# Performance work log

Measured on AMD Instinct MI355X. Metric: run time of the kernel, lower is better.

## Reference

```python
import jax, jax.numpy as jnp
import numpy as np

B, S, HID = 32, 577, 768
NH, HD = 12, 64  # num heads, head dim (HID = NH*HD)


def setup_inputs() -> dict:
    key = jax.random.key(0)
    ks = jax.random.split(key, 8)
    scale = 1.0 / np.sqrt(HID)
    return {
        "hidden_states": jax.random.normal(ks[0], (B, S, HID), jnp.float32),
        "lateral_states": jax.random.normal(ks[1], (B, NH, S, HD), jnp.float32),
        "Wq": jax.random.normal(ks[2], (HID, HID), jnp.float32) * scale,
        "bq": jax.random.normal(ks[3], (HID,), jnp.float32) * 0.02,
        "Wk": jax.random.normal(ks[4], (HID, HID), jnp.float32) * scale,
        "bk": jax.random.normal(ks[5], (HID,), jnp.float32) * 0.02,
        "Wv": jax.random.normal(ks[6], (HID, HID), jnp.float32) * scale,
        "bv": jax.random.normal(ks[7], (HID,), jnp.float32) * 0.02,
        "mix_with": 0,  # 0 -> 'q', 1 -> 'k', 2 -> 'v'
    }


def _heads(x):
    # [B, S, HID] -> [B, NH, S, HD]
    return x.reshape(B, S, NH, HD).transpose(0, 2, 1, 3)


def reference(hidden_states, lateral_states, Wq, bq, Wk, bk, Wv, bv, mix_with):
    q = _heads(hidden_states @ Wq.T + bq)
    k = _heads(hidden_states @ Wk.T + bk)
    v = _heads(hidden_states @ Wv.T + bv)
    if mix_with == 0:
        q = q * lateral_states
    elif mix_with == 1:
        k = k * lateral_states
    elif mix_with == 2:
        v = v * lateral_states
    else:
        raise ValueError("mix_with must be 0 (q), 1 (k), or 2 (v)")
    scores = jnp.einsum("bhqd,bhkd->bhqk", q, k) / jnp.sqrt(jnp.float32(HD))
    probs = jax.nn.softmax(scores, axis=-1)
    ctx = jnp.einsum("bhqk,bhkd->bhqd", probs, v)
    # [B, NH, S, HD] -> [B, S, HID]
    return ctx.transpose(0, 2, 1, 3).reshape(B, S, HID)
```

## Files before the change

kernel.cpp:

```cpp
#include <hip/hip_runtime.h>

#define B_    32
#define S_    577
#define HID_  768
#define NH_   12
#define HD_   64
#define SPAD  640
#define SB_   5
#define MT_   160
#define KT_   12
#define NT_   18

typedef __attribute__((ext_vector_type(8))) short short8;
typedef __attribute__((ext_vector_type(4))) short short4s;
typedef __attribute__((ext_vector_type(4))) float float4_;

static __device__ __forceinline__ float bf2f(short s) {
    union { float f; unsigned u; } cvt;
    cvt.u = ((unsigned)(unsigned short)s) << 16;
    return cvt.f;
}
static __device__ __forceinline__ short f2bf(float f) {
    union { float f; unsigned u; } cvt;
    cvt.f = f;
    unsigned u = cvt.u;
    unsigned r = u + 0x7FFF + ((u >> 16) & 1);
    return (short)(r >> 16);
}

__global__ __launch_bounds__(256) void convA_kernel(
    const float* __restrict__ X, short* __restrict__ ximg)
{
    const int mt = blockIdx.x, kt = blockIdx.y;
    const int b = mt / SB_, sb = mt - b * SB_;
    short* img = ximg + ((size_t)mt * KT_ + kt) * 8192;
#pragma unroll
    for (int i = 0; i < 4; ++i) {
        const int j = i * 256 + threadIdx.x;
        const int row = j >> 3, kg = j & 7;
        const int s = sb * 128 + row;
        const int srow = (s < S_) ? s : 0;
        const float* src = X + ((size_t)b * S_ + srow) * HID_ + kt * 64 + kg * 8;
        float4_ f0 = *(const float4_*)src;
        float4_ f1 = *(const float4_*)(src + 4);
        short8 s8;
#pragma unroll
        for (int e = 0; e < 4; ++e) { s8[e] = f2bf(f0[e]); s8[e + 4] = f2bf(f1[e]); }
        *(short8*)(img + ((size_t)kg * 128 + row) * 8) = s8;
    }
}

__global__ __launch_bounds__(256) void convB_kernel(
    const float* __restrict__ Wq, const float* __restrict__ Wk,
    const float* __restrict__ Wv, short* __restrict__ wimg)
{
    const int nt = blockIdx.x, kt = blockIdx.y;
    const int z = nt / 6;
    const float* W = (z == 0) ? Wq : (z == 1) ? Wk : Wv;
    const int n0 = (nt - z * 6) * 128;
    short* img = wimg + ((size_t)nt * KT_ + kt) * 8192;
#pragma unroll
    for (int i = 0; i < 4; ++i) {
        const int j = i * 256 + threadIdx.x;
        const int row = j >> 3, kg = j & 7;
        const float* src = W + (size_t)(n0 + row) * HID_ + kt * 64 + kg * 8;
        float4_ f0 = *(const float4_*)src;
        float4_ f1 = *(const float4_*)(src + 4);
        short8 s8;
#pragma unroll
        for (int e = 0; e < 4; ++e) { s8[e] = f2bf(f0[e]); s8[e + 4] = f2bf(f1[e]); }
        *(short8*)(img + ((size_t)kg * 128 + row) * 8) = s8;
    }
}

__global__ __launch_bounds__(256) void gemm_kernel(
    const short* __restrict__ ximg, const short* __restrict__ wimg,
    const float* __restrict__ bq, const float* __restrict__ bk,
    const float* __restrict__ bv,
    const float* __restrict__ lat, const int* __restrict__ mixw,
    short* __restrict__ qo, short* __restrict__ ko, short* __restrict__ vo)
{
    __shared__ __align__(16) short eP[4][4608];

    const int bid0 = blockIdx.x;
    const int bids = (bid0 & 7) * 360 + (bid0 >> 3);
    const int mt = bids / NT_;
    const int nt = bids - mt * NT_;

    const int z   = nt / 6;
    const int nz0 = (nt - z * 6) * 128;
    const int b   = mt / SB_;
    const int s0  = (mt - b * SB_) * 128;

    const int tid  = threadIdx.x;
    const int wave = tid >> 6;
    const int lane = tid & 63;
    const int quad = lane >> 4;
    const int l16  = lane & 15;

    const short* ag = ximg + ((size_t)mt * KT_) * 8192;
    const short* bg = wimg + ((size_t)nt * KT_) * 8192;

    float4_ acc[4][4] = {};
    const int r0 = (wave & 1) * 64 + l16;
    const int c0 = (wave >> 1) * 64 + l16;

    for (int kt = 0; kt < KT_; ++kt) {
        const short* ak = ag + (size_t)kt * 8192;
        const short* bk8p = bg + (size_t)kt * 8192;
#pragma unroll
        for (int c = 0; c < 2; ++c) {
            const int kb = (c * 4 + quad) * 128;
            short8 af[4], bf4[4];
#pragma unroll
            for (int mi = 0; mi < 4; ++mi)
                af[mi] = *(const short8*)(ak + (kb + r0 + mi * 16) * 8);
#pragma unroll
            for (int g = 0; g < 4; ++g)
                bf4[g] = *(const short8*)(bk8p + (kb + c0 + g * 16) * 8);
            __builtin_amdgcn_s_setprio(1);
#pragma unroll
            for (int mi = 0; mi < 4; ++mi)
#pragma unroll
                for (int g = 0; g < 4; ++g)
                    acc[mi][g] = __builtin_amdgcn_mfma_f32_16x16x32_bf16(
                        af[mi], bf4[g], acc[mi][g], 0, 0, 0);
            __builtin_amdgcn_s_setprio(0);
        }
    }

    const int mwv = *mixw;
    const float* bb = (z == 0) ? bq : (z == 1) ? bk : bv;
    const int hh   = (nz0 + (wave >> 1) * 64) >> 6;
    const size_t bh = (size_t)b * NH_ + hh;
    const int sW   = s0 + (wave & 1) * 64;
    const int ch   = sW >> 6;
    short* P = eP[wave];

    if (z < 2) {
#pragma unroll
        for (int mi = 0; mi < 4; ++mi)
#pragma unroll
            for (int i = 0; i < 4; ++i) {
                const int ml = mi * 16 + quad * 4 + i;
                const int s  = sW + ml;
                const float* lp =
                    lat + (bh * S_ + (s < S_ ? s : S_ - 1)) * HD_;
#pragma unroll
                for (int g = 0; g < 4; ++g) {
                    const int d = g * 16 + l16;
                    float val = acc[mi][g][i] + bb[hh * 64 + d];
                    if (z == mwv) val *= lp[d];
                    P[ml * 72 + d] = f2bf(val);
                }
            }
    } else {
#pragma unroll
        for (int mi = 0; mi < 4; ++mi)
#pragma unroll
            for (int g = 0; g < 4; ++g) {
                const int d  = g * 16 + l16;
                const int mb = mi * 16 + quad * 4;
                short4s w;
#pragma unroll
                for (int i = 0; i < 4; ++i) {
                    const int s = sW + mb + i;
                    float val = acc[mi][g][i] + bb[hh * 64 + d];
                    if (mwv == 2)
                        val *= lat[(bh * S_ + (s < S_ ? s : S_ - 1)) * HD_ + d];
                    w[i] = f2bf(val);
                }
                *(short4s*)(P + d * 72 + mb) = w;
            }
    }

    const int rr = lane >> 3, cc = lane & 7;
    if (z == 0) {
        short* qb = qo + (size_t)bh * SPAD * HD_;
#pragma unroll
        for (int j = 0; j < 8; ++j) {
            const int r = j * 8 + rr;
            *(short8*)(qb + (size_t)(sW + r) * 64 + cc * 8) =
                *(const short8*)(P + r * 72 + cc * 8);
        }
    } else if (z == 1) {
        short* kb_ = ko + ((size_t)bh * 10 + ch) * 4096;
#pragma unroll
        for (int j = 0; j < 8; ++j) {
            const int r = j * 8 + rr;
            *(short8*)(kb_ + (cc * 64 + r) * 8) =
                *(const short8*)(P + r * 72 + cc * 8);
        }
    } else {
        short* vb = vo + ((size_t)bh * 10 + ch) * 4096;
#pragma unroll
        for (int j = 0; j < 8; ++j) {
            const int r = j * 8 + rr;
            *(short8*)(vb + (cc * 64 + r) * 8) =
                *(const short8*)(P + r * 72 + cc * 8);
        }
    }
}

__global__ __launch_bounds__(256) void attn_kernel(
    const short* __restrict__ q, const short* __restrict__ k,
    const short* __restrict__ vt, float* __restrict__ out)
{
    __shared__ __align__(16) short pbuf[4][16][64];

    const int bid0 = blockIdx.x;
    const int bids = (bid0 & 7) * 480 + (bid0 >> 3);
    const int bh = bids / 10;
    const int qt = bids - bh * 10;

    const int b    = bh / NH_;
    const int h    = bh - b * NH_;
    const int tid  = threadIdx.x;
    const int wave = tid >> 6;
    const int lane = tid & 63;
    const int quad = lane >> 4;
    const int l16  = lane & 15;
    const int q0   = qt * 64 + wave * 16;

    const short* qp   = q  + (size_t)bh * SPAD * HD_;
    const short* kimg = k  + (size_t)bh * 40960;
    const short* vimg = vt + (size_t)bh * 40960;

    const short8 aq0 = *(const short8*)(qp + (size_t)(q0 + l16) * HD_ + quad * 8);
    const short8 aq1 = *(const short8*)(qp + (size_t)(q0 + l16) * HD_ + 32 + quad * 8);

    float m_i = -3.0e38f, l_i = 0.0f;
    float4_ O[4] = {};

    char* pw = (char*)&pbuf[wave][l16][0];
    const int swz = (l16 & 7) << 4;

    for (int kc = 0; kc < 10; ++kc) {
        const short* Kc = kimg + (size_t)kc * 4096;
        const short* Vc = vimg + (size_t)kc * 4096;

        float4_ sc[4] = {};
#pragma unroll
        for (int c = 0; c < 2; ++c) {
            const int kb = (c * 4 + quad) * 64;
            const short8 aq = c ? aq1 : aq0;
            short8 kf[4];
#pragma unroll
            for (int g = 0; g < 4; ++g)
                kf[g] = *(const short8*)(Kc + (kb + g * 16 + l16) * 8);
            __builtin_amdgcn_s_setprio(1);
#pragma unroll
            for (int g = 0; g < 4; ++g)
                sc[g] = __builtin_amdgcn_mfma_f32_16x16x32_bf16(kf[g], aq, sc[g], 0, 0, 0);
            __builtin_amdgcn_s_setprio(0);
        }

        if (kc == 9) {
#pragma unroll
            for (int g = 0; g < 4; ++g)
#pragma unroll
                for (int i = 0; i < 4; ++i)
                    if (576 + g * 16 + quad * 4 + i >= S_) sc[g][i] = -3.0e38f;
        }

        float cm = sc[0][0];
#pragma unroll
        for (int g = 0; g < 4; ++g)
#pragma unroll
            for (int i = 0; i < 4; ++i) cm = fmaxf(cm, sc[g][i]);
        cm = fmaxf(cm, __shfl_xor(cm, 16));
        cm = fmaxf(cm, __shfl_xor(cm, 32));

        const float mn    = fmaxf(m_i, cm);
        const float alpha = __expf((m_i - mn) * 0.125f);
        m_i = mn;
        const float mo = mn * 0.125f;

        float rs = 0.0f;
#pragma unroll
        for (int g = 0; g < 4; ++g) {
            short4s w;
#pragma unroll
            for (int i = 0; i < 4; ++i) {
                const float p = __expf(__builtin_fmaf(sc[g][i], 0.125f, -mo));
                const short pb = f2bf(p);
                w[i] = pb;
                rs += bf2f(pb);
            }
            *(short4s*)(pw + ((g * 32 + quad * 8) ^ swz)) = w;
        }
        rs += __shfl_xor(rs, 16);
        rs += __shfl_xor(rs, 32);
        l_i = l_i * alpha + rs;

        float av[4];
#pragma unroll
        for (int i = 0; i < 4; ++i)
            av[i] = __shfl(alpha, quad * 20 + i);
#pragma unroll
        for (int g = 0; g < 4; ++g)
#pragma unroll
            for (int i = 0; i < 4; ++i) O[g][i] *= av[i];

#pragma unroll
        for (int c = 0; c < 2; ++c) {
            const short8 ap =
                *(const short8*)(pw + ((c * 64 + quad * 16) ^ swz));
            const int kb = (c * 4 + quad) * 64;
            short8 vf[4];
#pragma unroll
            for (int g = 0; g < 4; ++g)
                vf[g] = *(const short8*)(Vc + (kb + g * 16 + l16) * 8);
            __builtin_amdgcn_s_setprio(1);
#pragma unroll
            for (int g = 0; g < 4; ++g)
                O[g] = __builtin_amdgcn_mfma_f32_16x16x32_bf16(ap, vf[g], O[g], 0, 0, 0);
            __builtin_amdgcn_s_setprio(0);
        }
    }

    float linv[4];
#pragma unroll
    for (int i = 0; i < 4; ++i)
        linv[i] = 1.0f / __shfl(l_i, quad * 20 + i);
#pragma unroll
    for (int i = 0; i < 4; ++i) {
        const int s = q0 + quad * 4 + i;
        if (s >= S_) continue;
#pragma unroll
        for (int g = 0; g < 4; ++g)
            out[((size_t)b * S_ + s) * HID_ + h * HD_ + g * 16 + l16] =
                O[g][i] * linv[i];
    }
}

extern "C" void kernel_launch(void* const* d_in, const int* in_sizes, int n_in,
                              void* d_out, int out_size, void* d_ws, size_t ws_size,
                              hipStream_t stream) {
    (void)in_sizes; (void)n_in; (void)out_size; (void)ws_size;

    const float* X   = (const float*)d_in[0];
    const float* lat = (const float*)d_in[1];
    const float* Wq  = (const float*)d_in[2];
    const float* bq  = (const float*)d_in[3];
    const float* Wk  = (const float*)d_in[4];
    const float* bk  = (const float*)d_in[5];
    const float* Wv  = (const float*)d_in[6];
    const float* bv  = (const float*)d_in[7];
    const int* mixw  = (const int*)d_in[8];
    float* out = (float*)d_out;

    const size_t per = (size_t)B_ * NH_ * SPAD * HD_;
    short* qw   = (short*)d_ws;
    short* kw   = qw + per;
    short* vw   = kw + per;
    short* wimg = vw + per;
    short* ximg = wimg + (size_t)NT_ * KT_ * 8192;

    convA_kernel<<<dim3(MT_, KT_), 256, 0, stream>>>(X, ximg);
    convB_kernel<<<dim3(NT_, KT_), 256, 0, stream>>>(Wq, Wk, Wv, wimg);
    gemm_kernel<<<dim3(2880), 256, 0, stream>>>(
        ximg, wimg, bq, bk, bv, lat, mixw, qw, kw, vw);
    attn_kernel<<<dim3(3840), 256, 0, stream>>>(qw, kw, vw, out);
}
```

Baseline: 386.9 us.

## Split GEMM blocks into 128-thread halves and use nontemporal loads/stores throughout

The QKV GEMM now launches 5760 blocks of two waves, each covering half the M rows of a 128x128 tile, so A/B tile reads are duplicated across the two blocks. The epilogue runs in two 32-row passes through a smaller LDS staging buffer, cutting LDS per block. Nontemporal loads and stores are added in the conversion kernels, the GEMM epilogue, and the attention Q loads and output stores to reduce cache pollution. Risks are doubled global traffic for the B operand and fewer waves per block for latency hiding.

```diff
diff --git a/kernel.cpp b/kernel.cpp
--- a/kernel.cpp
+++ b/kernel.cpp
@@ -41,12 +41,12 @@
         const int s = sb * 128 + row;
         const int srow = (s < S_) ? s : 0;
         const float* src = X + ((size_t)b * S_ + srow) * HID_ + kt * 64 + kg * 8;
-        float4_ f0 = *(const float4_*)src;
-        float4_ f1 = *(const float4_*)(src + 4);
+        float4_ f0 = __builtin_nontemporal_load((const float4_*)src);
+        float4_ f1 = __builtin_nontemporal_load((const float4_*)(src + 4));
         short8 s8;
 #pragma unroll
         for (int e = 0; e < 4; ++e) { s8[e] = f2bf(f0[e]); s8[e + 4] = f2bf(f1[e]); }
-        *(short8*)(img + ((size_t)kg * 128 + row) * 8) = s8;
+        __builtin_nontemporal_store(s8, (short8*)(img + ((size_t)kg * 128 + row) * 8));
     }
 }
 
@@ -64,28 +64,30 @@
         const int j = i * 256 + threadIdx.x;
         const int row = j >> 3, kg = j & 7;
         const float* src = W + (size_t)(n0 + row) * HID_ + kt * 64 + kg * 8;
-        float4_ f0 = *(const float4_*)src;
-        float4_ f1 = *(const float4_*)(src + 4);
+        float4_ f0 = __builtin_nontemporal_load((const float4_*)src);
+        float4_ f1 = __builtin_nontemporal_load((const float4_*)(src + 4));
         short8 s8;
 #pragma unroll
         for (int e = 0; e < 4; ++e) { s8[e] = f2bf(f0[e]); s8[e + 4] = f2bf(f1[e]); }
-        *(short8*)(img + ((size_t)kg * 128 + row) * 8) = s8;
-    }
-}
-
-__global__ __launch_bounds__(256) void gemm_kernel(
+        __builtin_nontemporal_store(s8, (short8*)(img + ((size_t)kg * 128 + row) * 8));
+    }
+}
+
+__global__ __launch_bounds__(128) void gemm_kernel(
     const short* __restrict__ ximg, const short* __restrict__ wimg,
     const float* __restrict__ bq, const float* __restrict__ bk,
     const float* __restrict__ bv,
     const float* __restrict__ lat, const int* __restrict__ mixw,
     short* __restrict__ qo, short* __restrict__ ko, short* __restrict__ vo)
 {
-    __shared__ __align__(16) short eP[4][4608];
+    __shared__ __align__(16) short eP[2][2560];
 
     const int bid0 = blockIdx.x;
-    const int bids = (bid0 & 7) * 360 + (bid0 >> 3);
-    const int mt = bids / NT_;
-    const int nt = bids - mt * NT_;
+    const int bids = (bid0 & 7) * 720 + (bid0 >> 3);
+    const int tile = bids >> 1;
+    const int wr   = bids & 1;
+    const int mt = tile / NT_;
+    const int nt = tile - mt * NT_;
 
     const int z   = nt / 6;
     const int nz0 = (nt - z * 6) * 128;
@@ -102,8 +104,8 @@
     const short* bg = wimg + ((size_t)nt * KT_) * 8192;
 
     float4_ acc[4][4] = {};
-    const int r0 = (wave & 1) * 64 + l16;
-    const int c0 = (wave >> 1) * 64 + l16;
+    const int r0 = wr * 64 + l16;
+    const int c0 = wave * 64 + l16;
 
     for (int kt = 0; kt < KT_; ++kt) {
         const short* ak = ag + (size_t)kt * 8192;
@@ -131,73 +133,83 @@
 
     const int mwv = *mixw;
     const float* bb = (z == 0) ? bq : (z == 1) ? bk : bv;
-    const int hh   = (nz0 + (wave >> 1) * 64) >> 6;
+    const int hh   = (nz0 + wave * 64) >> 6;
     const size_t bh = (size_t)b * NH_ + hh;
-    const int sW   = s0 + (wave & 1) * 64;
+    const int sW   = s0 + wr * 64;
     const int ch   = sW >> 6;
     short* P = eP[wave];
-
-    if (z < 2) {
-#pragma unroll
-        for (int mi = 0; mi < 4; ++mi)
-#pragma unroll
-            for (int i = 0; i < 4; ++i) {
-                const int ml = mi * 16 + quad * 4 + i;
-                const int s  = sW + ml;
-                const float* lp =
-                    lat + (bh * S_ + (s < S_ ? s : S_ - 1)) * HD_;
+    const int rr = lane >> 3, cc = lane & 7;
+
+#pragma unroll
+    for (int p = 0; p < 2; ++p) {
+        if (z < 2) {
+#pragma unroll
+            for (int mi2 = 0; mi2 < 2; ++mi2) {
+                const int mi = p * 2 + mi2;
+#pragma unroll
+                for (int i = 0; i < 4; ++i) {
+                    const int lr = mi2 * 16 + quad * 4 + i;
+                    const int s  = sW + p * 32 + lr;
+                    const float* lp =
+                        lat + (bh * S_ + (s < S_ ? s : S_ - 1)) * HD_;
+#pragma unroll
+                    for (int g = 0; g < 4; ++g) {
+                        const int d = g * 16 + l16;
+                        float val = acc[mi][g][i] + bb[hh * 64 + d];
+                        if (z == mwv) val *= __builtin_nontemporal_load(lp + d);
+                        P[lr * 72 + d] = f2bf(val);
+                    }
+                }
+            }
+            if (z == 0) {
+                short* qb = qo + (size_t)bh * SPAD * HD_;
+#pragma unroll
+                for (int j = 0; j < 4; ++j) {
+                    const int lr = j * 8 + rr;
+                    __builtin_nontemporal_store(
+                        *(const short8*)(P + lr * 72 + cc * 8),
+                        (short8*)(qb + (size_t)(sW + p * 32 + lr) * 64 + cc * 8));
+                }
+            } else {
+                short* kb_ = ko + ((size_t)bh * 10 + ch) * 4096;
+#pragma unroll
+                for (int j = 0; j < 4; ++j) {
+                    const int lr = j * 8 + rr;
+                    __builtin_nontemporal_store(
+                        *(const short8*)(P + lr * 72 + cc * 8),
+                        (short8*)(kb_ + (cc * 64 + p * 32 + lr) * 8));
+                }
+            }
+        } else {
+#pragma unroll
+            for (int mi2 = 0; mi2 < 2; ++mi2) {
+                const int mi = p * 2 + mi2;
+                const int lc = mi2 * 16 + quad * 4;
 #pragma unroll
                 for (int g = 0; g < 4; ++g) {
                     const int d = g * 16 + l16;
-                    float val = acc[mi][g][i] + bb[hh * 64 + d];
-                    if (z == mwv) val *= lp[d];
-                    P[ml * 72 + d] = f2bf(val);
+                    short4s w;
+#pragma unroll
+                    for (int i = 0; i < 4; ++i) {
+                        const int s = sW + p * 32 + lc + i;
+                        float val = acc[mi][g][i] + bb[hh * 64 + d];
+                        if (mwv == 2)
+                            val *= __builtin_nontemporal_load(
+                                lat + (bh * S_ + (s < S_ ? s : S_ - 1)) * HD_ + d);
+                        w[i] = f2bf(val);
+                    }
+                    *(short4s*)(P + d * 40 + lc) = w;
                 }
             }
-    } else {
-#pragma unroll
-        for (int mi = 0; mi < 4; ++mi)
-#pragma unroll
-            for (int g = 0; g < 4; ++g) {
-                const int d  = g * 16 + l16;
-                const int mb = mi * 16 + quad * 4;
-                short4s w;
-#pragma unroll
-                for (int i = 0; i < 4; ++i) {
-                    const int s = sW + mb + i;
-                    float val = acc[mi][g][i] + bb[hh * 64 + d];
-                    if (mwv == 2)
-                        val *= lat[(bh * S_ + (s < S_ ? s : S_ - 1)) * HD_ + d];
-                    w[i] = f2bf(val);
-                }
-                *(short4s*)(P + d * 72 + mb) = w;
-            }
-    }
-
-    const int rr = lane >> 3, cc = lane & 7;
-    if (z == 0) {
-        short* qb = qo + (size_t)bh * SPAD * HD_;
-#pragma unroll
-        for (int j = 0; j < 8; ++j) {
-            const int r = j * 8 + rr;
-            *(short8*)(qb + (size_t)(sW + r) * 64 + cc * 8) =
-                *(const short8*)(P + r * 72 + cc * 8);
-        }
-    } else if (z == 1) {
-        short* kb_ = ko + ((size_t)bh * 10 + ch) * 4096;
-#pragma unroll
-        for (int j = 0; j < 8; ++j) {
-            const int r = j * 8 + rr;
-            *(short8*)(kb_ + (cc * 64 + r) * 8) =
-                *(const short8*)(P + r * 72 + cc * 8);
-        }
-    } else {
-        short* vb = vo + ((size_t)bh * 10 + ch) * 4096;
-#pragma unroll
-        for (int j = 0; j < 8; ++j) {
-            const int r = j * 8 + rr;
-            *(short8*)(vb + (cc * 64 + r) * 8) =
-                *(const short8*)(P + r * 72 + cc * 8);
+            short* vb = vo + ((size_t)bh * 10 + ch) * 4096;
+#pragma unroll
+            for (int j = 0; j < 4; ++j) {
+                const int d   = j * 16 + (lane >> 2);
+                const int lc2 = lane & 3;
+                __builtin_nontemporal_store(
+                    *(const short8*)(P + d * 40 + lc2 * 8),
+                    (short8*)(vb + ((p * 4 + lc2) * 64 + d) * 8));
+            }
         }
     }
 }
@@ -226,8 +238,10 @@
     const short* kimg = k  + (size_t)bh * 40960;
     const short* vimg = vt + (size_t)bh * 40960;
 
-    const short8 aq0 = *(const short8*)(qp + (size_t)(q0 + l16) * HD_ + quad * 8);
-    const short8 aq1 = *(const short8*)(qp + (size_t)(q0 + l16) * HD_ + 32 + quad * 8);
+    const short8 aq0 = __builtin_nontemporal_load(
+        (const short8*)(qp + (size_t)(q0 + l16) * HD_ + quad * 8));
+    const short8 aq1 = __builtin_nontemporal_load(
+        (const short8*)(qp + (size_t)(q0 + l16) * HD_ + 32 + quad * 8));
 
     float m_i = -3.0e38f, l_i = 0.0f;
     float4_ O[4] = {};
@@ -329,8 +343,9 @@
         if (s >= S_) continue;
 #pragma unroll
         for (int g = 0; g < 4; ++g)
-            out[((size_t)b * S_ + s) * HID_ + h * HD_ + g * 16 + l16] =
-                O[g][i] * linv[i];
+            __builtin_nontemporal_store(
+                O[g][i] * linv[i],
+                out + ((size_t)b * S_ + s) * HID_ + h * HD_ + g * 16 + l16);
     }
 }
 
@@ -359,7 +374,7 @@
 
     convA_kernel<<<dim3(MT_, KT_), 256, 0, stream>>>(X, ximg);
     convB_kernel<<<dim3(NT_, KT_), 256, 0, stream>>>(Wq, Wk, Wv, wimg);
-    gemm_kernel<<<dim3(2880), 256, 0, stream>>>(
+    gemm_kernel<<<dim3(5760), 128, 0, stream>>>(
         ximg, wimg, bq, bk, bv, lat, mixw, qw, kw, vw);
     attn_kernel<<<dim3(3840), 256, 0, stream>>>(qw, kw, vw, out);
 }
```

After: 451.2 us. +16.6%, slower.
